# Performance work log

Hardware: AMD Instinct MI355X
Metric: run time of the kernel (lower is better)

Reference implementation:

```python
import jax, jax.numpy as jnp
import numpy as np

NB, D, ED, N, K, DTR = 4, 1024, 2048, 32, 4, 64
B, L = 1, 1024


def setup_inputs():
    key = jax.random.key(0)
    ks = jax.random.split(key, 10)
    g = lambda k, s, sc=0.02: jax.random.normal(k, s, dtype=jnp.float32) * sc
    A_log = jnp.log(jnp.broadcast_to(jnp.arange(1, N + 1, dtype=jnp.float32), (NB, ED, N))) + 0.0
    return {
        "x": g(ks[0], (B, L, D), 1.0),
        "Wi": g(ks[1], (D, D)),
        "bi": jnp.zeros((D,), jnp.float32),
        "ln_g": jnp.ones((NB, D), jnp.float32),
        "ln_b": jnp.zeros((NB, D), jnp.float32),
        "in_w": g(ks[2], (NB, 2 * ED, D)),
        "conv_w": g(ks[3], (NB, ED, 1, K), 0.2),
        "conv_b": jnp.zeros((NB, ED), jnp.float32),
        "xproj_w": g(ks[4], (NB, DTR + 2 * N, ED)),
        "dtproj_w": g(ks[5], (NB, ED, DTR), 0.1),
        "dtproj_b": jnp.full((NB, ED), -4.0, jnp.float32),
        "A_log": A_log,
        "Dp": jnp.ones((NB, ED), jnp.float32),
        "out_w": g(ks[6], (NB, D, ED)),
        "fn_g": jnp.ones((D,), jnp.float32),
        "fn_b": jnp.zeros((D,), jnp.float32),
        "sp_w": g(ks[7], (N, D)),
        "sp_b": jnp.zeros((N,), jnp.float32),
    }


def layernorm(x, g, b, eps=1e-5):
    m = jnp.mean(x, axis=-1, keepdims=True)
    v = jnp.mean(jnp.square(x - m), axis=-1, keepdims=True)
    return (x - m) * jax.lax.rsqrt(v + eps) * g + b


def mamba(u_in, in_w, conv_w, conv_b, xproj_w, dtproj_w, dtproj_b, A_log, Dp, out_w):
    # u_in: (B, L, D)
    xz = u_in @ in_w.T                       # (B, L, 2*ED)
    u, z = jnp.split(xz, 2, axis=-1)         # each (B, L, ED)
    # causal depthwise conv over time
    uc = jnp.swapaxes(u, 1, 2)               # (B, ED, L)
    uc = jax.lax.conv_general_dilated(uc, conv_w, (1,), [(K - 1, 0)], feature_group_count=ED)
    uc = uc + conv_b[None, :, None]
    u = jax.nn.silu(jnp.swapaxes(uc, 1, 2))  # (B, L, ED)
    x_dbl = u @ xproj_w.T                    # (B, L, DTR + 2N)
    dt, Bm, Cm = jnp.split(x_dbl, [DTR, DTR + N], axis=-1)
    delta = jax.nn.softplus(dt @ dtproj_w.T + dtproj_b)  # (B, L, ED)
    A = -jnp.exp(A_log)                                  # (ED, N)
    dA = jnp.exp(delta[..., None] * A)                   # (B, L, ED, N)
    dBu = (delta * u)[..., None] * Bm[:, :, None, :]     # (B, L, ED, N)

    def step(h, inp):
        dA_t, dBu_t, C_t = inp
        h = dA_t * h + dBu_t
        y = jnp.einsum('ben,bn->be', h, C_t)
        return h, y

    h0 = jnp.zeros((u.shape[0], ED, N), u.dtype)
    _, ys = jax.lax.scan(step, h0, (jnp.swapaxes(dA, 0, 1), jnp.swapaxes(dBu, 0, 1), jnp.swapaxes(Cm, 0, 1)))
    y = jnp.swapaxes(ys, 0, 1) + u * Dp      # (B, L, ED)
    y = y * jax.nn.silu(z)
    return y @ out_w.T                       # (B, L, D)


def reference(x, Wi, bi, ln_g, ln_b, in_w, conv_w, conv_b, xproj_w, dtproj_w, dtproj_b, A_log, Dp, out_w, fn_g, fn_b, sp_w, sp_b):
    h = x @ Wi.T + bi
    for i in range(NB):
        normed = layernorm(h, ln_g[i], ln_b[i])
        h = h + mamba(normed, in_w[i], conv_w[i], conv_b[i], xproj_w[i],
                      dtproj_w[i], dtproj_b[i], A_log[i], Dp[i], out_w[i])
    h = layernorm(h, fn_g, fn_b)
    state = jnp.mean(h, axis=1) @ sp_w.T + sp_b   # (B, N)
    return h, state
```

## Files before the change

### kernel.cpp

```cpp
#include <hip/hip_runtime.h>
#include <math.h>

#define D_    1024
#define ED_   2048
#define NST   32
#define KCONV 4
#define DTR_  64
#define L_    1024
#define NB_   4
#define NCH   8
#define CHUNK (L_ / NCH)
#define KSPL  8
#define ZSPL  4

typedef __bf16 bf16_8 __attribute__((ext_vector_type(8)));
typedef __bf16 bf16_4 __attribute__((ext_vector_type(4)));
typedef float  f32x4  __attribute__((ext_vector_type(4)));

__device__ __forceinline__ float softplus_f(float x) {
  return x > 20.f ? x : log1pf(expf(x));
}
__device__ __forceinline__ float silu_f(float x) {
  return x / (1.f + expf(-x));
}

__global__ __launch_bounds__(256) void f2bf_k(
    const float* __restrict__ in, __bf16* __restrict__ out, int n)
{
  const int i = (blockIdx.x * 256 + threadIdx.x) * 8;
  if (i >= n) return;
  const float4 a = *reinterpret_cast<const float4*>(in + i);
  const float4 b = *reinterpret_cast<const float4*>(in + i + 4);
  bf16_8 v;
  v[0]=(__bf16)a.x; v[1]=(__bf16)a.y; v[2]=(__bf16)a.z; v[3]=(__bf16)a.w;
  v[4]=(__bf16)b.x; v[5]=(__bf16)b.y; v[6]=(__bf16)b.z; v[7]=(__bf16)b.w;
  *reinterpret_cast<bf16_8*>(out + i) = v;
}

__global__ __launch_bounds__(256) void gemm_mfma(
    const __bf16* __restrict__ A, int lda,
    const __bf16* __restrict__ W, int ldw,
    const float* __restrict__ bias, float* __restrict__ C, int ldc,
    int K, int flags)
{
  __shared__ __bf16 As[128 * 32];
  __shared__ __bf16 Ws[128 * 32];
  const int tid  = threadIdx.x;
  const int lane = tid & 63;
  const int w    = tid >> 6;
  const int wr   = w >> 1, wc = w & 1;
  const int row0 = blockIdx.y * 128, col0 = blockIdx.x * 128;

  f32x4 acc[4][4] = {};

  for (int k0 = 0; k0 < K; k0 += 32) {
    #pragma unroll
    for (int j = 0; j < 2; ++j) {
      const int inst = w * 2 + j;
      const int eo   = inst * 512 + lane * 8;
      const int r    = eo >> 5, k = eo & 31;
      __builtin_amdgcn_global_load_lds(
          (const __attribute__((address_space(1))) void*)(A + (size_t)(row0 + r) * lda + k0 + k),
          (__attribute__((address_space(3))) void*)(&As[inst * 512]), 16, 0, 0);
      __builtin_amdgcn_global_load_lds(
          (const __attribute__((address_space(1))) void*)(W + (size_t)(col0 + r) * ldw + k0 + k),
          (__attribute__((address_space(3))) void*)(&Ws[inst * 512]), 16, 0, 0);
    }
    __syncthreads();
    bf16_8 af[4], bfr[4];
    const int kk  = (lane >> 4) * 8;
    const int r16 = lane & 15;
    #pragma unroll
    for (int m = 0; m < 4; ++m)
      af[m] = *reinterpret_cast<const bf16_8*>(&As[(wr * 64 + m * 16 + r16) * 32 + kk]);
    #pragma unroll
    for (int n = 0; n < 4; ++n)
      bfr[n] = *reinterpret_cast<const bf16_8*>(&Ws[(wc * 64 + n * 16 + r16) * 32 + kk]);
    #pragma unroll
    for (int m = 0; m < 4; ++m)
      #pragma unroll
      for (int n = 0; n < 4; ++n)
        acc[m][n] = __builtin_amdgcn_mfma_f32_16x16x32_bf16(af[m], bfr[n], acc[m][n], 0, 0, 0);
    __syncthreads();
  }

  const int crow = (lane >> 4) * 4;
  const int ccol = lane & 15;
  #pragma unroll
  for (int m = 0; m < 4; ++m)
    #pragma unroll
    for (int n = 0; n < 4; ++n) {
      const int col = col0 + wc * 64 + n * 16 + ccol;
      const float bv = (flags & 4) ? bias[col] : 0.f;
      #pragma unroll
      for (int r = 0; r < 4; ++r) {
        const int row = row0 + wr * 64 + m * 16 + crow + r;
        float* cp = C + (size_t)row * ldc + col;
        float v = acc[m][n][r] + bv;
        if (flags & 2) v = softplus_f(v);
        if (flags & 1) v += *cp;
        *cp = v;
      }
    }
}

__global__ __launch_bounds__(256) void gemm_mfma_sk(
    const __bf16* __restrict__ A, const __bf16* __restrict__ W,
    float* __restrict__ partials, int M, int N, int K, int Kc)
{
  __shared__ __bf16 As[128 * 32];
  __shared__ __bf16 Ws[128 * 32];
  const int tid  = threadIdx.x;
  const int lane = tid & 63;
  const int w    = tid >> 6;
  const int wr   = w >> 1, wc = w & 1;
  const int row0 = blockIdx.y * 128, col0 = blockIdx.x * 128;
  const int kbase = blockIdx.z * Kc;

  f32x4 acc[4][4] = {};

  for (int k0 = kbase; k0 < kbase + Kc; k0 += 32) {
    #pragma unroll
    for (int j = 0; j < 2; ++j) {
      const int inst = w * 2 + j;
      const int eo   = inst * 512 + lane * 8;
      const int r    = eo >> 5, k = eo & 31;
      __builtin_amdgcn_global_load_lds(
          (const __attribute__((address_space(1))) void*)(A + (size_t)(row0 + r) * K + k0 + k),
          (__attribute__((address_space(3))) void*)(&As[inst * 512]), 16, 0, 0);
      __builtin_amdgcn_global_load_lds(
          (const __attribute__((address_space(1))) void*)(W + (size_t)(col0 + r) * K + k0 + k),
          (__attribute__((address_space(3))) void*)(&Ws[inst * 512]), 16, 0, 0);
    }
    __syncthreads();
    bf16_8 af[4], bfr[4];
    const int kk  = (lane >> 4) * 8;
    const int r16 = lane & 15;
    #pragma unroll
    for (int m = 0; m < 4; ++m)
      af[m] = *reinterpret_cast<const bf16_8*>(&As[(wr * 64 + m * 16 + r16) * 32 + kk]);
    #pragma unroll
    for (int n = 0; n < 4; ++n)
      bfr[n] = *reinterpret_cast<const bf16_8*>(&Ws[(wc * 64 + n * 16 + r16) * 32 + kk]);
    #pragma unroll
    for (int m = 0; m < 4; ++m)
      #pragma unroll
      for (int n = 0; n < 4; ++n)
        acc[m][n] = __builtin_amdgcn_mfma_f32_16x16x32_bf16(af[m], bfr[n], acc[m][n], 0, 0, 0);
    __syncthreads();
  }

  float* base = partials + (size_t)blockIdx.z * M * N;
  const int crow = (lane >> 4) * 4;
  const int ccol = lane & 15;
  #pragma unroll
  for (int m = 0; m < 4; ++m)
    #pragma unroll
    for (int n = 0; n < 4; ++n) {
      const int col = col0 + wc * 64 + n * 16 + ccol;
      #pragma unroll
      for (int r = 0; r < 4; ++r) {
        const int row = row0 + wr * 64 + m * 16 + crow + r;
        base[(size_t)row * N + col] = acc[m][n][r];
      }
    }
}

__global__ __launch_bounds__(256) void mfma_sk_reduce(
    const float* __restrict__ partials, const float* __restrict__ bias,
    float* __restrict__ C, int elems, int ncols, int flags)
{
  const int i = (blockIdx.x * 256 + threadIdx.x) * 4;
  if (i >= elems) return;
  float4 s = *reinterpret_cast<const float4*>(partials + i);
  #pragma unroll
  for (int z = 1; z < ZSPL; ++z) {
    const float4 p = *reinterpret_cast<const float4*>(partials + (size_t)z * elems + i);
    s.x += p.x; s.y += p.y; s.z += p.z; s.w += p.w;
  }
  if (flags & 4) {
    const float4 bv = *reinterpret_cast<const float4*>(bias + (i % ncols));
    s.x += bv.x; s.y += bv.y; s.z += bv.z; s.w += bv.w;
  }
  if (flags & 1) {
    const float4 ov = *reinterpret_cast<const float4*>(C + i);
    s.x += ov.x; s.y += ov.y; s.z += ov.z; s.w += ov.w;
  }
  *reinterpret_cast<float4*>(C + i) = s;
}

__global__ __launch_bounds__(256) void gemm_bt_sk(
    const float* __restrict__ A, int lda,
    const float* __restrict__ W, int ldw,
    float* __restrict__ partials, int ldc,
    int M, int N, int K)
{
  __shared__ float As[16][65];
  __shared__ float Ws[16][65];
  const int tid = threadIdx.x;
  const int row0 = blockIdx.y * 64, col0 = blockIdx.x * 64;
  const int Kc = K / KSPL;
  const int kbase = blockIdx.z * Kc;
  const int tx = tid & 15, ty = tid >> 4;
  const int lm = tid >> 2, lk = (tid & 3) << 2;
  float acc[4][4] = {};
  for (int k0 = kbase; k0 < kbase + Kc; k0 += 16) {
    float4 av = *reinterpret_cast<const float4*>(A + (size_t)(row0 + lm) * lda + k0 + lk);
    float4 wv = *reinterpret_cast<const float4*>(W + (size_t)(col0 + lm) * ldw + k0 + lk);
    __syncthreads();
    As[lk+0][lm]=av.x; As[lk+1][lm]=av.y; As[lk+2][lm]=av.z; As[lk+3][lm]=av.w;
    Ws[lk+0][lm]=wv.x; Ws[lk+1][lm]=wv.y; Ws[lk+2][lm]=wv.z; Ws[lk+3][lm]=wv.w;
    __syncthreads();
    #pragma unroll
    for (int k = 0; k < 16; ++k) {
      float a0 = As[k][ty*4+0], a1 = As[k][ty*4+1], a2 = As[k][ty*4+2], a3 = As[k][ty*4+3];
      float b0 = Ws[k][tx*4+0], b1 = Ws[k][tx*4+1], b2 = Ws[k][tx*4+2], b3 = Ws[k][tx*4+3];
      acc[0][0] += a0*b0; acc[0][1] += a0*b1; acc[0][2] += a0*b2; acc[0][3] += a0*b3;
      acc[1][0] += a1*b0; acc[1][1] += a1*b1; acc[1][2] += a1*b2; acc[1][3] += a1*b3;
      acc[2][0] += a2*b0; acc[2][1] += a2*b1; acc[2][2] += a2*b2; acc[2][3] += a2*b3;
      acc[3][0] += a3*b0; acc[3][1] += a3*b1; acc[3][2] += a3*b2; acc[3][3] += a3*b3;
    }
  }
  float* base = partials + (size_t)blockIdx.z * M * ldc;
  #pragma unroll
  for (int i = 0; i < 4; ++i) {
    const int r = row0 + ty*4 + i;
    float4 v = make_float4(acc[i][0], acc[i][1], acc[i][2], acc[i][3]);
    *reinterpret_cast<float4*>(base + (size_t)r * ldc + col0 + tx*4) = v;
  }
}

__global__ __launch_bounds__(256) void sk_reduce_k(
    const float* __restrict__ partials, float* __restrict__ C,
    __bf16* __restrict__ Cbf, int elems)
{
  const int i = (blockIdx.x * 256 + threadIdx.x) * 4;
  if (i >= elems) return;
  float4 s = *reinterpret_cast<const float4*>(partials + i);
  #pragma unroll
  for (int z = 1; z < KSPL; ++z) {
    const float4 p = *reinterpret_cast<const float4*>(partials + (size_t)z * elems + i);
    s.x += p.x; s.y += p.y; s.z += p.z; s.w += p.w;
  }
  *reinterpret_cast<float4*>(C + i) = s;
  bf16_4 b;
  b[0]=(__bf16)s.x; b[1]=(__bf16)s.y; b[2]=(__bf16)s.z; b[3]=(__bf16)s.w;
  *reinterpret_cast<bf16_4*>(Cbf + i) = b;
}

__global__ __launch_bounds__(256) void layernorm_k(
    const float* __restrict__ x, const float* __restrict__ g,
    const float* __restrict__ b, float* __restrict__ out)
{
  __shared__ float red[8];
  const int row = blockIdx.x;
  const int tid = threadIdx.x;
  const float* xr = x + (size_t)row * D_;
  float4 v = *reinterpret_cast<const float4*>(xr + tid * 4);
  float s = v.x + v.y + v.z + v.w;
  #pragma unroll
  for (int off = 32; off; off >>= 1) s += __shfl_down(s, off, 64);
  if ((tid & 63) == 0) red[tid >> 6] = s;
  __syncthreads();
  const float m = (red[0] + red[1] + red[2] + red[3]) * (1.f / D_);
  float dx0 = v.x - m, dx1 = v.y - m, dx2 = v.z - m, dx3 = v.w - m;
  float ss = dx0*dx0 + dx1*dx1 + dx2*dx2 + dx3*dx3;
  #pragma unroll
  for (int off = 32; off; off >>= 1) ss += __shfl_down(ss, off, 64);
  if ((tid & 63) == 0) red[4 + (tid >> 6)] = ss;
  __syncthreads();
  const float var = (red[4] + red[5] + red[6] + red[7]) * (1.f / D_);
  const float rs = rsqrtf(var + 1e-5f);
  const int c = tid * 4;
  const float4 gv = *reinterpret_cast<const float4*>(g + c);
  const float4 bv = *reinterpret_cast<const float4*>(b + c);
  float4 o;
  o.x = dx0 * rs * gv.x + bv.x;
  o.y = dx1 * rs * gv.y + bv.y;
  o.z = dx2 * rs * gv.z + bv.z;
  o.w = dx3 * rs * gv.w + bv.w;
  *reinterpret_cast<float4*>(out + (size_t)row * D_ + c) = o;
}

__global__ __launch_bounds__(256) void layernorm_bf_k(
    const float* __restrict__ x, const float* __restrict__ g,
    const float* __restrict__ b, __bf16* __restrict__ out)
{
  __shared__ float red[8];
  const int row = blockIdx.x;
  const int tid = threadIdx.x;
  const float* xr = x + (size_t)row * D_;
  float4 v = *reinterpret_cast<const float4*>(xr + tid * 4);
  float s = v.x + v.y + v.z + v.w;
  #pragma unroll
  for (int off = 32; off; off >>= 1) s += __shfl_down(s, off, 64);
  if ((tid & 63) == 0) red[tid >> 6] = s;
  __syncthreads();
  const float m = (red[0] + red[1] + red[2] + red[3]) * (1.f / D_);
  float dx0 = v.x - m, dx1 = v.y - m, dx2 = v.z - m, dx3 = v.w - m;
  float ss = dx0*dx0 + dx1*dx1 + dx2*dx2 + dx3*dx3;
  #pragma unroll
  for (int off = 32; off; off >>= 1) ss += __shfl_down(ss, off, 64);
  if ((tid & 63) == 0) red[4 + (tid >> 6)] = ss;
  __syncthreads();
  const float var = (red[4] + red[5] + red[6] + red[7]) * (1.f / D_);
  const float rs = rsqrtf(var + 1e-5f);
  const int c = tid * 4;
  const float4 gv = *reinterpret_cast<const float4*>(g + c);
  const float4 bv = *reinterpret_cast<const float4*>(b + c);
  bf16_4 o;
  o[0] = (__bf16)(dx0 * rs * gv.x + bv.x);
  o[1] = (__bf16)(dx1 * rs * gv.y + bv.y);
  o[2] = (__bf16)(dx2 * rs * gv.z + bv.z);
  o[3] = (__bf16)(dx3 * rs * gv.w + bv.w);
  *reinterpret_cast<bf16_4*>(out + (size_t)row * D_ + c) = o;
}

__global__ __launch_bounds__(256) void conv_silu_k(
    const float* __restrict__ xz, const float* __restrict__ cw,
    const float* __restrict__ cb, float* __restrict__ u)
{
  const int e = blockIdx.x * 256 + threadIdx.x;
  const int t0 = blockIdx.y * 8;
  const float w0 = cw[e*4+0], w1 = cw[e*4+1], w2 = cw[e*4+2], w3 = cw[e*4+3];
  const float b = cb[e];
  float x0 = (t0 >= 3) ? xz[(size_t)(t0-3)*(2*ED_)+e] : 0.f;
  float x1 = (t0 >= 2) ? xz[(size_t)(t0-2)*(2*ED_)+e] : 0.f;
  float x2 = (t0 >= 1) ? xz[(size_t)(t0-1)*(2*ED_)+e] : 0.f;
  #pragma unroll
  for (int j = 0; j < 8; ++j) {
    const float x3 = xz[(size_t)(t0+j)*(2*ED_)+e];
    const float acc = b + w0*x0 + w1*x1 + w2*x2 + w3*x3;
    u[(size_t)(t0+j)*ED_+e] = silu_f(acc);
    x0 = x1; x1 = x2; x2 = x3;
  }
}

__global__ __launch_bounds__(256) void scan_phase1(
    const float* __restrict__ delta, const float* __restrict__ u,
    const float* __restrict__ xdbl, const float* __restrict__ A_log,
    float* __restrict__ hend, float* __restrict__ Pend)
{
  __shared__ float dl[16][8], ul[16][8];
  __shared__ float bl[16][32];
  const int tid = threadIdx.x;
  const int n = tid & 31;
  const int c = tid >> 5;
  const int e0 = blockIdx.x * 8;
  const int e = e0 + c;
  const int ch = blockIdx.y;
  const float a = -expf(A_log[e * NST + n]);
  float h = 0.f, S = 0.f;
  const int t0 = ch * CHUNK;
  const int s_t = (tid & 127) >> 3, s_e = tid & 7;
  const int b_c = (tid & 7) * 4;

  float rg_a = 0.f;
  float4 rg_b;
  if (tid < 128) {
    rg_a = delta[(size_t)(t0 + s_t) * ED_ + e0 + s_e];
    rg_b = *reinterpret_cast<const float4*>(&xdbl[(size_t)(t0 + s_t) * 128 + 64 + b_c]);
  } else {
    rg_a = u[(size_t)(t0 + s_t) * ED_ + e0 + s_e];
  }

  for (int tb = 0; tb < CHUNK; tb += 16) {
    if (tid < 128) {
      dl[s_t][s_e] = rg_a;
      *reinterpret_cast<float4*>(&bl[s_t][b_c]) = rg_b;
    } else {
      ul[s_t][s_e] = rg_a;
    }
    __syncthreads();
    if (tb + 16 < CHUNK) {
      const int t = t0 + tb + 16 + s_t;
      if (tid < 128) {
        rg_a = delta[(size_t)t * ED_ + e0 + s_e];
        rg_b = *reinterpret_cast<const float4*>(&xdbl[(size_t)t * 128 + 64 + b_c]);
      } else {
        rg_a = u[(size_t)t * ED_ + e0 + s_e];
      }
    }
    #pragma unroll
    for (int j = 0; j < 16; ++j) {
      const float sd = dl[j][c];
      const float uv = ul[j][c];
      const float Bv = bl[j][n];
      h = fmaf(__expf(sd * a), h, sd * uv * Bv);
      S += sd;
    }
    __syncthreads();
  }
  const int idx = ch * (ED_ * NST) + blockIdx.x * 256 + tid;
  hend[idx] = h;
  Pend[idx] = __expf(a * S);
}

__global__ __launch_bounds__(256, 7) void scan_phase3(
    const float* __restrict__ delta, const float* __restrict__ u,
    const float* __restrict__ xdbl, const float* __restrict__ A_log,
    const float* __restrict__ hend, const float* __restrict__ Pend,
    const float* __restrict__ Dp,
    const float* __restrict__ xz, __bf16* __restrict__ y)
{
  __shared__ float p_lds[8][16][33];
  __shared__ float dl[16][8], ul[16][8], zl[16][8];
  __shared__ float bc[16][64];
  const int tid = threadIdx.x;
  const int n = tid & 31;
  const int c = tid >> 5;
  const int e0 = blockIdx.x * 8;
  const int e = e0 + c;
  const int ch = blockIdx.y;
  const float a = -expf(A_log[e * NST + n]);
  const float dp = Dp[e];

  float h = 0.f;
  {
    const int sidx = blockIdx.x * 256 + tid;
    for (int cc = 0; cc < ch; ++cc) {
      const int off = cc * (ED_ * NST) + sidx;
      h = fmaf(Pend[off], h, hend[off]);
    }
  }

  const int t0 = ch * CHUNK;
  const int r = n & 15, half = n >> 4;
  const int s_t  = (tid & 127) >> 3;
  const int s_e  = tid & 7;
  const int b_t  = tid >> 4;
  const int b_c  = (tid & 15) * 4;

  float rg_a = 0.f, rg_z = 0.f;
  float4 rg_bc;
  {
    const int t = t0 + s_t;
    if (tid < 128) {
      rg_a = delta[(size_t)t * ED_ + e0 + s_e];
      rg_z = xz[(size_t)t * (2*ED_) + ED_ + e0 + s_e];
    } else {
      rg_a = u[(size_t)t * ED_ + e0 + s_e];
    }
    rg_bc = *reinterpret_cast<const float4*>(&xdbl[(size_t)(t0 + b_t) * 128 + 64 + b_c]);
  }

  for (int tb = 0; tb < CHUNK; tb += 16) {
    if (tid < 128) { dl[s_t][s_e] = rg_a; zl[s_t][s_e] = rg_z; }
    else          { ul[s_t][s_e] = rg_a; }
    *reinterpret_cast<float4*>(&bc[b_t][b_c]) = rg_bc;
    __syncthreads();
    if (tb + 16 < CHUNK) {
      const int t = t0 + tb + 16 + s_t;
      if (tid < 128) {
        rg_a = delta[(size_t)t * ED_ + e0 + s_e];
        rg_z = xz[(size_t)t * (2*ED_) + ED_ + e0 + s_e];
      } else {
        rg_a = u[(size_t)t * ED_ + e0 + s_e];
      }
      rg_bc = *reinterpret_cast<const float4*>(&xdbl[(size_t)(t0 + tb + 16 + b_t) * 128 + 64 + b_c]);
    }
    #pragma unroll
    for (int j = 0; j < 16; ++j) {
      const float sd = dl[j][c];
      const float uv = ul[j][c];
      const float Bv = bc[j][n];
      const float Cv = bc[j][32 + n];
      const float dA = __expf(sd * a);
      h = fmaf(dA, h, sd * uv * Bv);
      p_lds[c][j][n] = h * Cv;
    }
    __syncthreads();
    float s = 0.f;
    #pragma unroll
    for (int k = 0; k < 16; ++k) s += p_lds[c][r][half * 16 + k];
    s += __shfl_xor(s, 16, 64);
    if (half == 0) {
      const float uvt = ul[r][c];
      const float zv  = zl[r][c];
      y[(size_t)(t0 + tb + r) * ED_ + e] = (__bf16)((s + uvt * dp) * silu_f(zv));
    }
    __syncthreads();
  }
}

__global__ __launch_bounds__(256) void colmean_part_k(
    const float* __restrict__ hf, float* __restrict__ part)
{
  const int d = blockIdx.x * 256 + threadIdx.x;
  const int tc = blockIdx.y;
  float s = 0.f;
  #pragma unroll 8
  for (int j = 0; j < 32; ++j) s += hf[(size_t)(tc * 32 + j) * D_ + d];
  part[tc * D_ + d] = s;
}

__global__ __launch_bounds__(256) void colmean_fin_k(
    const float* __restrict__ part, float* __restrict__ cm)
{
  const int d = blockIdx.x * 256 + threadIdx.x;
  float s = 0.f;
  #pragma unroll
  for (int c = 0; c < 32; ++c) s += part[c * D_ + d];
  cm[d] = s * (1.f / L_);
}

__global__ __launch_bounds__(256) void state_k(
    const float* __restrict__ cm, const float* __restrict__ spw,
    const float* __restrict__ spb, float* __restrict__ out)
{
  __shared__ float red[4];
  const int nidx = blockIdx.x;
  const int tid = threadIdx.x;
  float s = 0.f;
  for (int d = tid; d < D_; d += 256) s += cm[d] * spw[(size_t)nidx * D_ + d];
  #pragma unroll
  for (int off = 32; off; off >>= 1) s += __shfl_down(s, off, 64);
  if ((tid & 63) == 0) red[tid >> 6] = s;
  __syncthreads();
  if (tid == 0) out[nidx] = red[0] + red[1] + red[2] + red[3] + spb[nidx];
}

extern "C" void kernel_launch(void* const* d_in, const int* in_sizes, int n_in,
                              void* d_out, int out_size, void* d_ws, size_t ws_size,
                              hipStream_t stream) {
  const float* x        = (const float*)d_in[0];
  const float* Wi       = (const float*)d_in[1];
  const float* bi       = (const float*)d_in[2];
  const float* ln_g     = (const float*)d_in[3];
  const float* ln_b     = (const float*)d_in[4];
  const float* in_w     = (const float*)d_in[5];
  const float* conv_w   = (const float*)d_in[6];
  const float* conv_b   = (const float*)d_in[7];
  const float* xproj_w  = (const float*)d_in[8];
  const float* dtproj_w = (const float*)d_in[9];
  const float* dtproj_b = (const float*)d_in[10];
  const float* A_log    = (const float*)d_in[11];
  const float* Dp       = (const float*)d_in[12];
  const float* out_w    = (const float*)d_in[13];
  const float* fn_g     = (const float*)d_in[14];
  const float* fn_b     = (const float*)d_in[15];
  const float* sp_w     = (const float*)d_in[16];
  const float* sp_b     = (const float*)d_in[17];
  float* out  = (float*)d_out;
  float* ws_f = (float*)d_ws;

  float* h_buf  = ws_f;
  float* xz     = ws_f + 1048576;
  float* u_buf  = ws_f + 5242880;
  float* xdbl   = ws_f + 7340032;
  float* delta  = ws_f + 7471104;
  float* hend   = ws_f + 9568256;
  float* pend   = ws_f + 10092544;
  float* cmean  = ws_f + 10616832;
  __bf16* nbf   = (__bf16*)(ws_f + 10617856);
  __bf16* ybf   = (__bf16*)(ws_f + 11142144);
  __bf16* wbf   = (__bf16*)(ws_f + 12190720);
  __bf16* xdblbf= (__bf16*)(ws_f + 16385024);
  __bf16* dtwbf = (__bf16*)(ws_f + 16450560);
  float* skpart = hend;
  float* skmf   = u_buf;
  float* cmpart = hend;

  const dim3 blk(256);

  f2bf_k<<<512, blk, 0, stream>>>(x, nbf, L_ * D_);
  f2bf_k<<<512, blk, 0, stream>>>(Wi, wbf, D_ * D_);
  gemm_mfma_sk<<<dim3(D_/128, L_/128, ZSPL), blk, 0, stream>>>(
      nbf, wbf, skmf, L_, D_, D_, D_/ZSPL);
  mfma_sk_reduce<<<dim3(L_*D_/4/256), blk, 0, stream>>>(
      skmf, bi, h_buf, L_*D_, D_, 4);

  for (int i = 0; i < NB_; ++i) {
    layernorm_bf_k<<<L_, blk, 0, stream>>>(h_buf, ln_g + i*D_, ln_b + i*D_, nbf);
    f2bf_k<<<2048, blk, 0, stream>>>(in_w + (size_t)i*2*ED_*D_, wbf, 2*ED_*D_);
    gemm_mfma<<<dim3(2*ED_/128, L_/128), blk, 0, stream>>>(
        nbf, D_, wbf, D_, nullptr, xz, 2*ED_, D_, 0);
    conv_silu_k<<<dim3(ED_/256, L_/8), blk, 0, stream>>>(
        xz, conv_w + (size_t)i*ED_*KCONV, conv_b + (size_t)i*ED_, u_buf);
    gemm_bt_sk<<<dim3(128/64, L_/64, KSPL), blk, 0, stream>>>(
        u_buf, ED_, xproj_w + (size_t)i*128*ED_, ED_, skpart, 128, L_, 128, ED_);
    sk_reduce_k<<<dim3(L_*128/4/256), blk, 0, stream>>>(skpart, xdbl, xdblbf, L_ * 128);
    f2bf_k<<<64, blk, 0, stream>>>(dtproj_w + (size_t)i*ED_*DTR_, dtwbf, ED_*DTR_);
    gemm_mfma<<<dim3(ED_/128, L_/128), blk, 0, stream>>>(
        xdblbf, 128, dtwbf, DTR_, dtproj_b + (size_t)i*ED_, delta, ED_, DTR_, 2 | 4);
    scan_phase1<<<dim3(ED_/8, NCH), blk, 0, stream>>>(
        delta, u_buf, xdbl, A_log + (size_t)i*ED_*NST, hend, pend);
    scan_phase3<<<dim3(ED_/8, NCH), blk, 0, stream>>>(
        delta, u_buf, xdbl, A_log + (size_t)i*ED_*NST, hend, pend,
        Dp + (size_t)i*ED_, xz, ybf);
    f2bf_k<<<1024, blk, 0, stream>>>(out_w + (size_t)i*D_*ED_, wbf, D_*ED_);
    gemm_mfma_sk<<<dim3(D_/128, L_/128, ZSPL), blk, 0, stream>>>(
        ybf, wbf, skmf, L_, D_, ED_, ED_/ZSPL);
    mfma_sk_reduce<<<dim3(L_*D_/4/256), blk, 0, stream>>>(
        skmf, nullptr, h_buf, L_*D_, D_, 1);
  }

  layernorm_k<<<L_, blk, 0, stream>>>(h_buf, fn_g, fn_b, out);
  colmean_part_k<<<dim3(D_/256, 32), blk, 0, stream>>>(out, cmpart);
  colmean_fin_k<<<D_/256, blk, 0, stream>>>(cmpart, cmean);
  state_k<<<NST, blk, 0, stream>>>(cmean, sp_w, sp_b, out + (size_t)L_*D_);
}
```

Measured before the change: 712.9 us.

## Widen MFMA GEMM K-tile with swizzled LDS and move x_proj to bf16 MFMA

```diff
diff --git a/kernel.cpp b/kernel.cpp
--- a/kernel.cpp
+++ b/kernel.cpp
@@ -10,8 +10,8 @@
 #define NB_   4
 #define NCH   8
 #define CHUNK (L_ / NCH)
-#define KSPL  8
 #define ZSPL  4
+#define XPZ   16
 
 typedef __bf16 bf16_8 __attribute__((ext_vector_type(8)));
 typedef __bf16 bf16_4 __attribute__((ext_vector_type(4)));
@@ -43,8 +43,8 @@
     const float* __restrict__ bias, float* __restrict__ C, int ldc,
     int K, int flags)
 {
-  __shared__ __bf16 As[128 * 32];
-  __shared__ __bf16 Ws[128 * 32];
+  __shared__ __bf16 As[128 * 64];
+  __shared__ __bf16 Ws[128 * 64];
   const int tid  = threadIdx.x;
   const int lane = tid & 63;
   const int w    = tid >> 6;
@@ -53,34 +53,43 @@
 
   f32x4 acc[4][4] = {};
 
-  for (int k0 = 0; k0 < K; k0 += 32) {
-    #pragma unroll
-    for (int j = 0; j < 2; ++j) {
-      const int inst = w * 2 + j;
-      const int eo   = inst * 512 + lane * 8;
-      const int r    = eo >> 5, k = eo & 31;
+  for (int k0 = 0; k0 < K; k0 += 64) {
+    #pragma unroll
+    for (int j = 0; j < 4; ++j) {
+      const int inst = w * 4 + j;
+      const int row  = inst * 8 + (lane >> 3);
+      const int lu   = (lane & 7) ^ (row & 7);
       __builtin_amdgcn_global_load_lds(
-          (const __attribute__((address_space(1))) void*)(A + (size_t)(row0 + r) * lda + k0 + k),
+          (const __attribute__((address_space(1))) void*)(A + (size_t)(row0 + row) * lda + k0 + lu * 8),
           (__attribute__((address_space(3))) void*)(&As[inst * 512]), 16, 0, 0);
       __builtin_amdgcn_global_load_lds(
-          (const __attribute__((address_space(1))) void*)(W + (size_t)(col0 + r) * ldw + k0 + k),
+          (const __attribute__((address_space(1))) void*)(W + (size_t)(col0 + row) * ldw + k0 + lu * 8),
           (__attribute__((address_space(3))) void*)(&Ws[inst * 512]), 16, 0, 0);
     }
     __syncthreads();
-    bf16_8 af[4], bfr[4];
-    const int kk  = (lane >> 4) * 8;
     const int r16 = lane & 15;
-    #pragma unroll
-    for (int m = 0; m < 4; ++m)
-      af[m] = *reinterpret_cast<const bf16_8*>(&As[(wr * 64 + m * 16 + r16) * 32 + kk]);
-    #pragma unroll
-    for (int n = 0; n < 4; ++n)
-      bfr[n] = *reinterpret_cast<const bf16_8*>(&Ws[(wc * 64 + n * 16 + r16) * 32 + kk]);
-    #pragma unroll
-    for (int m = 0; m < 4; ++m)
-      #pragma unroll
-      for (int n = 0; n < 4; ++n)
-        acc[m][n] = __builtin_amdgcn_mfma_f32_16x16x32_bf16(af[m], bfr[n], acc[m][n], 0, 0, 0);
+    const int uq  = lane >> 4;
+    #pragma unroll
+    for (int ks = 0; ks < 2; ++ks) {
+      bf16_8 af[4], bfr[4];
+      #pragma unroll
+      for (int m = 0; m < 4; ++m) {
+        const int row = wr * 64 + m * 16 + r16;
+        const int pu  = (ks * 4 + uq) ^ (row & 7);
+        af[m] = *reinterpret_cast<const bf16_8*>(&As[row * 64 + pu * 8]);
+      }
+      #pragma unroll
+      for (int n = 0; n < 4; ++n) {
+        const int row = wc * 64 + n * 16 + r16;
+        const int pu  = (ks * 4 + uq) ^ (row & 7);
+        bfr[n] = *reinterpret_cast<const bf16_8*>(&Ws[row * 64 + pu * 8]);
+      }
+      #pragma unroll
+      for (int m = 0; m < 4; ++m)
+        #pragma unroll
+        for (int n = 0; n < 4; ++n)
+          acc[m][n] = __builtin_amdgcn_mfma_f32_16x16x32_bf16(af[m], bfr[n], acc[m][n], 0, 0, 0);
+    }
     __syncthreads();
   }
 
@@ -108,8 +117,8 @@
     const __bf16* __restrict__ A, const __bf16* __restrict__ W,
     float* __restrict__ partials, int M, int N, int K, int Kc)
 {
-  __shared__ __bf16 As[128 * 32];
-  __shared__ __bf16 Ws[128 * 32];
+  __shared__ __bf16 As[128 * 64];
+  __shared__ __bf16 Ws[128 * 64];
   const int tid  = threadIdx.x;
   const int lane = tid & 63;
   const int w    = tid >> 6;
@@ -119,34 +128,43 @@
 
   f32x4 acc[4][4] = {};
 
-  for (int k0 = kbase; k0 < kbase + Kc; k0 += 32) {
-    #pragma unroll
-    for (int j = 0; j < 2; ++j) {
-      const int inst = w * 2 + j;
-      const int eo   = inst * 512 + lane * 8;
-      const int r    = eo >> 5, k = eo & 31;
+  for (int k0 = kbase; k0 < kbase + Kc; k0 += 64) {
+    #pragma unroll
+    for (int j = 0; j < 4; ++j) {
+      const int inst = w * 4 + j;
+      const int row  = inst * 8 + (lane >> 3);
+      const int lu   = (lane & 7) ^ (row & 7);
       __builtin_amdgcn_global_load_lds(
-          (const __attribute__((address_space(1))) void*)(A + (size_t)(row0 + r) * K + k0 + k),
+          (const __attribute__((address_space(1))) void*)(A + (size_t)(row0 + row) * K + k0 + lu * 8),
           (__attribute__((address_space(3))) void*)(&As[inst * 512]), 16, 0, 0);
       __builtin_amdgcn_global_load_lds(
-          (const __attribute__((address_space(1))) void*)(W + (size_t)(col0 + r) * K + k0 + k),
+          (const __attribute__((address_space(1))) void*)(W + (size_t)(col0 + row) * K + k0 + lu * 8),
           (__attribute__((address_space(3))) void*)(&Ws[inst * 512]), 16, 0, 0);
     }
     __syncthreads();
-    bf16_8 af[4], bfr[4];
-    const int kk  = (lane >> 4) * 8;
     const int r16 = lane & 15;
-    #pragma unroll
-    for (int m = 0; m < 4; ++m)
-      af[m] = *reinterpret_cast<const bf16_8*>(&As[(wr * 64 + m * 16 + r16) * 32 + kk]);
-    #pragma unroll
-    for (int n = 0; n < 4; ++n)
-      bfr[n] = *reinterpret_cast<const bf16_8*>(&Ws[(wc * 64 + n * 16 + r16) * 32 + kk]);
-    #pragma unroll
-    for (int m = 0; m < 4; ++m)
-      #pragma unroll
-      for (int n = 0; n < 4; ++n)
-        acc[m][n] = __builtin_amdgcn_mfma_f32_16x16x32_bf16(af[m], bfr[n], acc[m][n], 0, 0, 0);
+    const int uq  = lane >> 4;
+    #pragma unroll
+    for (int ks = 0; ks < 2; ++ks) {
+      bf16_8 af[4], bfr[4];
+      #pragma unroll
+      for (int m = 0; m < 4; ++m) {
+        const int row = wr * 64 + m * 16 + r16;
+        const int pu  = (ks * 4 + uq) ^ (row & 7);
+        af[m] = *reinterpret_cast<const bf16_8*>(&As[row * 64 + pu * 8]);
+      }
+      #pragma unroll
+      for (int n = 0; n < 4; ++n) {
+        const int row = wc * 64 + n * 16 + r16;
+        const int pu  = (ks * 4 + uq) ^ (row & 7);
+        bfr[n] = *reinterpret_cast<const bf16_8*>(&Ws[row * 64 + pu * 8]);
+      }
+      #pragma unroll
+      for (int m = 0; m < 4; ++m)
+        #pragma unroll
+        for (int n = 0; n < 4; ++n)
+          acc[m][n] = __builtin_amdgcn_mfma_f32_16x16x32_bf16(af[m], bfr[n], acc[m][n], 0, 0, 0);
+    }
     __syncthreads();
   }
 
@@ -168,13 +186,13 @@
 
 __global__ __launch_bounds__(256) void mfma_sk_reduce(
     const float* __restrict__ partials, const float* __restrict__ bias,
-    float* __restrict__ C, int elems, int ncols, int flags)
+    float* __restrict__ C, __bf16* __restrict__ Cbf,
+    int elems, int ncols, int nz, int flags)
 {
   const int i = (blockIdx.x * 256 + threadIdx.x) * 4;
   if (i >= elems) return;
   float4 s = *reinterpret_cast<const float4*>(partials + i);
-  #pragma unroll
-  for (int z = 1; z < ZSPL; ++z) {
+  for (int z = 1; z < nz; ++z) {
     const float4 p = *reinterpret_cast<const float4*>(partials + (size_t)z * elems + i);
     s.x += p.x; s.y += p.y; s.z += p.z; s.w += p.w;
   }
@@ -187,65 +205,11 @@
     s.x += ov.x; s.y += ov.y; s.z += ov.z; s.w += ov.w;
   }
   *reinterpret_cast<float4*>(C + i) = s;
-}
-
-__global__ __launch_bounds__(256) void gemm_bt_sk(
-    const float* __restrict__ A, int lda,
-    const float* __restrict__ W, int ldw,
-    float* __restrict__ partials, int ldc,
-    int M, int N, int K)
-{
-  __shared__ float As[16][65];
-  __shared__ float Ws[16][65];
-  const int tid = threadIdx.x;
-  const int row0 = blockIdx.y * 64, col0 = blockIdx.x * 64;
-  const int Kc = K / KSPL;
-  const int kbase = blockIdx.z * Kc;
-  const int tx = tid & 15, ty = tid >> 4;
-  const int lm = tid >> 2, lk = (tid & 3) << 2;
-  float acc[4][4] = {};
-  for (int k0 = kbase; k0 < kbase + Kc; k0 += 16) {
-    float4 av = *reinterpret_cast<const float4*>(A + (size_t)(row0 + lm) * lda + k0 + lk);
-    float4 wv = *reinterpret_cast<const float4*>(W + (size_t)(col0 + lm) * ldw + k0 + lk);
-    __syncthreads();
-    As[lk+0][lm]=av.x; As[lk+1][lm]=av.y; As[lk+2][lm]=av.z; As[lk+3][lm]=av.w;
-    Ws[lk+0][lm]=wv.x; Ws[lk+1][lm]=wv.y; Ws[lk+2][lm]=wv.z; Ws[lk+3][lm]=wv.w;
-    __syncthreads();
-    #pragma unroll
-    for (int k = 0; k < 16; ++k) {
-      float a0 = As[k][ty*4+0], a1 = As[k][ty*4+1], a2 = As[k][ty*4+2], a3 = As[k][ty*4+3];
-      float b0 = Ws[k][tx*4+0], b1 = Ws[k][tx*4+1], b2 = Ws[k][tx*4+2], b3 = Ws[k][tx*4+3];
-      acc[0][0] += a0*b0; acc[0][1] += a0*b1; acc[0][2] += a0*b2; acc[0][3] += a0*b3;
-      acc[1][0] += a1*b0; acc[1][1] += a1*b1; acc[1][2] += a1*b2; acc[1][3] += a1*b3;
-      acc[2][0] += a2*b0; acc[2][1] += a2*b1; acc[2][2] += a2*b2; acc[2][3] += a2*b3;
-      acc[3][0] += a3*b0; acc[3][1] += a3*b1; acc[3][2] += a3*b2; acc[3][3] += a3*b3;
-    }
-  }
-  float* base = partials + (size_t)blockIdx.z * M * ldc;
-  #pragma unroll
-  for (int i = 0; i < 4; ++i) {
-    const int r = row0 + ty*4 + i;
-    float4 v = make_float4(acc[i][0], acc[i][1], acc[i][2], acc[i][3]);
-    *reinterpret_cast<float4*>(base + (size_t)r * ldc + col0 + tx*4) = v;
-  }
-}
-
-__global__ __launch_bounds__(256) void sk_reduce_k(
-    const float* __restrict__ partials, float* __restrict__ C,
-    __bf16* __restrict__ Cbf, int elems)
-{
-  const int i = (blockIdx.x * 256 + threadIdx.x) * 4;
-  if (i >= elems) return;
-  float4 s = *reinterpret_cast<const float4*>(partials + i);
-  #pragma unroll
-  for (int z = 1; z < KSPL; ++z) {
-    const float4 p = *reinterpret_cast<const float4*>(partials + (size_t)z * elems + i);
-    s.x += p.x; s.y += p.y; s.z += p.z; s.w += p.w;
-  }
-  *reinterpret_cast<float4*>(C + i) = s;
-  bf16_4 b;
-  b[0]=(__bf16)s.x; b[1]=(__bf16)s.y; b[2]=(__bf16)s.z; b[3]=(__bf16)s.w;
-  *reinterpret_cast<bf16_4*>(Cbf + i) = b;
+  if (flags & 8) {
+    bf16_4 b;
+    b[0]=(__bf16)s.x; b[1]=(__bf16)s.y; b[2]=(__bf16)s.z; b[3]=(__bf16)s.w;
+    *reinterpret_cast<bf16_4*>(Cbf + i) = b;
+  }
 }
 
 __global__ __launch_bounds__(256) void layernorm_k(
@@ -318,7 +282,7 @@
 
 __global__ __launch_bounds__(256) void conv_silu_k(
     const float* __restrict__ xz, const float* __restrict__ cw,
-    const float* __restrict__ cb, float* __restrict__ u)
+    const float* __restrict__ cb, float* __restrict__ u, __bf16* __restrict__ ub)
 {
   const int e = blockIdx.x * 256 + threadIdx.x;
   const int t0 = blockIdx.y * 8;
@@ -330,8 +294,9 @@
   #pragma unroll
   for (int j = 0; j < 8; ++j) {
     const float x3 = xz[(size_t)(t0+j)*(2*ED_)+e];
-    const float acc = b + w0*x0 + w1*x1 + w2*x2 + w3*x3;
-    u[(size_t)(t0+j)*ED_+e] = silu_f(acc);
+    const float uv = silu_f(b + w0*x0 + w1*x1 + w2*x2 + w3*x3);
+    u[(size_t)(t0+j)*ED_+e] = uv;
+    ub[(size_t)(t0+j)*ED_+e] = (__bf16)uv;
     x0 = x1; x1 = x2; x2 = x3;
   }
 }
@@ -557,8 +522,10 @@
   __bf16* wbf   = (__bf16*)(ws_f + 12190720);
   __bf16* xdblbf= (__bf16*)(ws_f + 16385024);
   __bf16* dtwbf = (__bf16*)(ws_f + 16450560);
-  float* skpart = hend;
+  __bf16* ubf   = (__bf16*)(ws_f + 16516096);
+  __bf16* xpbf  = (__bf16*)(ws_f + 17564672);
   float* skmf   = u_buf;
+  float* skxp   = delta;
   float* cmpart = hend;
 
   const dim3 blk(256);
@@ -568,7 +535,7 @@
   gemm_mfma_sk<<<dim3(D_/128, L_/128, ZSPL), blk, 0, stream>>>(
       nbf, wbf, skmf, L_, D_, D_, D_/ZSPL);
   mfma_sk_reduce<<<dim3(L_*D_/4/256), blk, 0, stream>>>(
-      skmf, bi, h_buf, L_*D_, D_, 4);
+      skmf, bi, h_buf, nullptr, L_*D_, D_, ZSPL, 4);
 
   for (int i = 0; i < NB_; ++i) {
     layernorm_bf_k<<<L_, blk, 0, stream>>>(h_buf, ln_g + i*D_, ln_b + i*D_, nbf);
@@ -576,10 +543,12 @@
     gemm_mfma<<<dim3(2*ED_/128, L_/128), blk, 0, stream>>>(
         nbf, D_, wbf, D_, nullptr, xz, 2*ED_, D_, 0);
     conv_silu_k<<<dim3(ED_/256, L_/8), blk, 0, stream>>>(
-        xz, conv_w + (size_t)i*ED_*KCONV, conv_b + (size_t)i*ED_, u_buf);
-    gemm_bt_sk<<<dim3(128/64, L_/64, KSPL), blk, 0, stream>>>(
-        u_buf, ED_, xproj_w + (size_t)i*128*ED_, ED_, skpart, 128, L_, 128, ED_);
-    sk_reduce_k<<<dim3(L_*128/4/256), blk, 0, stream>>>(skpart, xdbl, xdblbf, L_ * 128);
+        xz, conv_w + (size_t)i*ED_*KCONV, conv_b + (size_t)i*ED_, u_buf, ubf);
+    f2bf_k<<<128, blk, 0, stream>>>(xproj_w + (size_t)i*128*ED_, xpbf, 128*ED_);
+    gemm_mfma_sk<<<dim3(1, L_/128, XPZ), blk, 0, stream>>>(
+        ubf, xpbf, skxp, L_, 128, ED_, ED_/XPZ);
+    mfma_sk_reduce<<<dim3(L_*128/4/256), blk, 0, stream>>>(
+        skxp, nullptr, xdbl, xdblbf, L_*128, 128, XPZ, 8);
     f2bf_k<<<64, blk, 0, stream>>>(dtproj_w + (size_t)i*ED_*DTR_, dtwbf, ED_*DTR_);
     gemm_mfma<<<dim3(ED_/128, L_/128), blk, 0, stream>>>(
         xdblbf, 128, dtwbf, DTR_, dtproj_b + (size_t)i*ED_, delta, ED_, DTR_, 2 | 4);
@@ -592,7 +561,7 @@
     gemm_mfma_sk<<<dim3(D_/128, L_/128, ZSPL), blk, 0, stream>>>(
         ybf, wbf, skmf, L_, D_, ED_, ED_/ZSPL);
     mfma_sk_reduce<<<dim3(L_*D_/4/256), blk, 0, stream>>>(
-        skmf, nullptr, h_buf, L_*D_, D_, 1);
+        skmf, nullptr, h_buf, nullptr, L_*D_, D_, ZSPL, 1);
   }
 
   layernorm_k<<<L_, blk, 0, stream>>>(h_buf, fn_g, fn_b, out);
```

Result: faster. 673.6 us (-5.5%).
